# Kernel optimization log

Measured on AMD Instinct MI355X. Metric: run time of the kernel, lower is better.

Reference implementation:

```python
import jax, jax.numpy as jnp
import numpy as np


def setup_inputs() -> dict:
    key = jax.random.key(0)
    ks = jax.random.split(key, 7)
    n, L = 8, 1024
    s = 64            # input_size_1 = input_size_2 = 64
    d = s + 1         # 65, after bias-ones concat / h feature size
    inp = {
        "layer1": jax.random.normal(ks[0], (n, L, s), dtype=jnp.float32),
        "layer2": jax.random.normal(ks[1], (n, L, s), dtype=jnp.float32),
        "layer3": jax.random.normal(ks[2], (n, L, s), dtype=jnp.float32),
        "h1": jax.random.normal(ks[3], (n, L, d), dtype=jnp.float32),
        "h2": jax.random.normal(ks[4], (n, L, d), dtype=jnp.float32),
        "h3": jax.random.normal(ks[5], (n, L, d), dtype=jnp.float32),
        # quartic core W (xavier-normal-ish scale): shape (s1+1, s2+1, s2+1, s2+1)
        "W": jax.random.normal(ks[6], (d, d, d, d), dtype=jnp.float32) * 0.02,
    }
    return inp


def reference(layer1, layer2, layer3, h1, h2, h3, W):
    # Non-factorized, flag=True, 3D-input path of Qriaffine.forward:
    #   out = einsum('nia,abcd,njb,nic,njd->nij', [layer1;1], W, [layer2;1], h1, h2)
    # layer3 / h3 are unused in this branch (but layer3 is still concatenated
    # with ones in the original code, a no-op for the output).
    n, L, _ = layer1.shape
    ones = jnp.ones((n, L, 1), dtype=layer1.dtype)
    l1 = jnp.concatenate([layer1, ones], axis=-1)  # [n, L, d]
    l2 = jnp.concatenate([layer2, ones], axis=-1)  # [n, L, d]
    # efficient contraction order, avoiding the huge [n,L,d,d,d] intermediate:
    p = l1[..., :, None] * h1[..., None, :]          # niac: [n, L, d, d]
    q = jnp.einsum('niac,abcd->nibd', p, W)          # [n, L, d, d]
    r = l2[..., :, None] * h2[..., None, :]          # njbd: [n, L, d, d]
    out = jnp.einsum('nibd,njbd->nij', q, r)         # [n, L, L]
    return out
```

## Files before the change

kernel.cpp:

```cpp
#include <hip/hip_runtime.h>
#include <hip/hip_bf16.h>


typedef __attribute__((ext_vector_type(8))) short short8;
typedef __attribute__((ext_vector_type(16))) float floatx16;

#define KP 4288
#define DP 4352
#define NROW 8192

__device__ __forceinline__ void async_ld16(const void* g, void* l) {
  __builtin_amdgcn_global_load_lds(
      (const __attribute__((address_space(1))) unsigned int*)g,
      (__attribute__((address_space(3))) unsigned int*)l, 16, 0, 0);
}

__global__ void zero_pad_wt2(__hip_bfloat16* __restrict__ Wt2) {
  const int ROWPAD = 127 * KP;
  const int COLPAD = 4225 * 63;
  const int total = ROWPAD + COLPAD;
  const __hip_bfloat16 z = __float2bfloat16(0.f);
  for (int id = blockIdx.x * 256 + threadIdx.x; id < total;
       id += gridDim.x * 256) {
    if (id < ROWPAD) {
      int row = 4225 + id / KP, col = id % KP;
      Wt2[(size_t)row * KP + col] = z;
    } else {
      int j = id - ROWPAD;
      int row = j / 63, col = 4225 + j % 63;
      Wt2[(size_t)row * KP + col] = z;
    }
  }
}

__global__ void build_wt2(const float* __restrict__ W, __hip_bfloat16* __restrict__ Wt2) {
  __shared__ __hip_bfloat16 tile[65 * 66];
  const int a = blockIdx.x, b = blockIdx.y;
  const float* src = W + (size_t)(a * 65 + b) * 4225;
  for (int idx = threadIdx.x; idx < 4225; idx += 256) {
    int c = idx / 65, d = idx - c * 65;
    tile[d * 66 + c] = __float2bfloat16(src[idx]);
  }
  __syncthreads();
  for (int idx = threadIdx.x; idx < 4225; idx += 256) {
    int d = idx / 65, c = idx - d * 65;
    Wt2[(size_t)(b * 65 + d) * KP + a * 65 + c] = tile[d * 66 + c];
  }
}

__global__ void build_p(const float* __restrict__ layer, const float* __restrict__ h,
                        __hip_bfloat16* __restrict__ P, int width) {
  const int row0 = blockIdx.x * 4;
  __shared__ float lv[4][65], hv[4][65];
  for (int i = threadIdx.x; i < 260; i += 256) {
    int rr = i / 65, x = i - rr * 65;
    lv[rr][x] = (x < 64) ? layer[(size_t)(row0 + rr) * 64 + x] : 1.0f;
    hv[rr][x] = h[(size_t)(row0 + rr) * 65 + x];
  }
  __syncthreads();
#pragma unroll
  for (int rr = 0; rr < 4; ++rr) {
    const size_t rowbase = (size_t)(row0 + rr) * width;
    for (int base = threadIdx.x * 8; base < width; base += 256 * 8) {
      alignas(16) __hip_bfloat16 tmp[8];
#pragma unroll
      for (int j = 0; j < 8; ++j) {
        int idx = base + j;
        float v = 0.f;
        if (idx < 4225) {
          int x = idx / 65, y = idx - x * 65;
          v = lv[rr][x] * hv[rr][y];
        }
        tmp[j] = __float2bfloat16(v);
      }
      *(float4*)(P + rowbase + base) = *(const float4*)tmp;
    }
  }
}

template <int STORE_BF16, int SWZ>
__global__ __launch_bounds__(256) void gemm_nt(
    const __hip_bfloat16* __restrict__ A, const __hip_bfloat16* __restrict__ B,
    void* __restrict__ Cv, int K, int lda, int ldb, int ldc,
    long sA, long sB, long sC) {
  __shared__ alignas(16) __hip_bfloat16 As[128 * 64];
  __shared__ alignas(16) __hip_bfloat16 Bs[128 * 64];
  int bx = blockIdx.x, by = blockIdx.y, z = blockIdx.z;
  if (SWZ == 1) {
    int orig = blockIdx.x + 34 * blockIdx.y;
    int xcd = orig & 7;
    int idx = orig >> 3;
    int xg = (idx < 216) ? (idx / 72) : 3;
    int r = idx - xg * 72;
    bx = xg * 9 + (r >> 3);
    by = (xcd << 3) + (r & 7);
  } else if (SWZ == 2) {
    int orig = blockIdx.x + 8 * blockIdx.y + 64 * blockIdx.z;
    z = orig & 7;
    int r = orig >> 3;
    bx = r & 7;
    by = r >> 3;
  }
  A += (long)z * sA;
  B += (long)z * sB;
  const int bm = by * 128;
  const int bn = bx * 128;
  const int t = threadIdx.x;
  const int lane = t & 63;
  const int wave = t >> 6;
  const int l31 = lane & 31;
  const int lhi = lane >> 5;
  const int wm = (wave >> 1) * 64;
  const int wn = (wave & 1) * 64;

  const __hip_bfloat16* gA[4];
  const __hip_bfloat16* gB[4];
  __hip_bfloat16* lA[4];
  __hip_bfloat16* lB[4];
#pragma unroll
  for (int r = 0; r < 4; ++r) {
    int L = r * 256 + t;
    int row = L >> 3, sl = L & 7;
    int sg = sl ^ (row & 7);
    gA[r] = A + (size_t)(bm + row) * lda + sg * 8;
    gB[r] = B + (size_t)(bn + row) * ldb + sg * 8;
    lA[r] = As + (size_t)(r * 256 + wave * 64) * 8;
    lB[r] = Bs + (size_t)(r * 256 + wave * 64) * 8;
  }

  const int x7 = l31 & 7;
  const int rA0 = (wm + l31) * 64, rA1 = (wm + 32 + l31) * 64;
  const int rB0 = (wn + l31) * 64, rB1 = (wn + 32 + l31) * 64;

  floatx16 acc[2][2] = {};

  for (int k0 = 0; k0 < K; k0 += 64) {
    __syncthreads();
#pragma unroll
    for (int r = 0; r < 4; ++r) {
      async_ld16(gA[r] + k0, lA[r]);
      async_ld16(gB[r] + k0, lB[r]);
    }
    __syncthreads();

#pragma unroll
    for (int ks = 0; ks < 4; ++ks) {
      const int pc = ((ks * 2 + lhi) ^ x7) * 8;
      short8 a0 = *(const short8*)(&As[rA0 + pc]);
      short8 a1 = *(const short8*)(&As[rA1 + pc]);
      short8 b0 = *(const short8*)(&Bs[rB0 + pc]);
      short8 b1 = *(const short8*)(&Bs[rB1 + pc]);
      acc[0][0] = __builtin_amdgcn_mfma_f32_32x32x16_bf16(a0, b0, acc[0][0], 0, 0, 0);
      acc[0][1] = __builtin_amdgcn_mfma_f32_32x32x16_bf16(a0, b1, acc[0][1], 0, 0, 0);
      acc[1][0] = __builtin_amdgcn_mfma_f32_32x32x16_bf16(a1, b0, acc[1][0], 0, 0, 0);
      acc[1][1] = __builtin_amdgcn_mfma_f32_32x32x16_bf16(a1, b1, acc[1][1], 0, 0, 0);
    }
  }

  if (STORE_BF16) {
    __hip_bfloat16* C = (__hip_bfloat16*)Cv + (long)z * sC;
#pragma unroll
    for (int mt = 0; mt < 2; ++mt)
#pragma unroll
      for (int nt = 0; nt < 2; ++nt)
#pragma unroll
        for (int reg = 0; reg < 16; ++reg) {
          int row = bm + wm + mt * 32 + (reg & 3) + 8 * (reg >> 2) + 4 * lhi;
          int col = bn + wn + nt * 32 + l31;
          C[(size_t)row * ldc + col] = __float2bfloat16(acc[mt][nt][reg]);
        }
  } else {
    float* C = (float*)Cv + (long)z * sC;
#pragma unroll
    for (int mt = 0; mt < 2; ++mt)
#pragma unroll
      for (int nt = 0; nt < 2; ++nt)
#pragma unroll
        for (int reg = 0; reg < 16; ++reg) {
          int row = bm + wm + mt * 32 + (reg & 3) + 8 * (reg >> 2) + 4 * lhi;
          int col = bn + wn + nt * 32 + l31;
          C[(size_t)row * ldc + col] = acc[mt][nt][reg];
        }
  }
}

extern "C" void kernel_launch(void* const* d_in, const int* in_sizes, int n_in,
                              void* d_out, int out_size, void* d_ws, size_t ws_size,
                              hipStream_t stream) {
  const float* layer1 = (const float*)d_in[0];
  const float* layer2 = (const float*)d_in[1];
  const float* h1 = (const float*)d_in[3];
  const float* h2 = (const float*)d_in[4];
  const float* W = (const float*)d_in[6];
  float* out = (float*)d_out;

  char* ws = (char*)d_ws;
  __hip_bfloat16* P = (__hip_bfloat16*)(ws);
  __hip_bfloat16* Wt2 = (__hip_bfloat16*)(ws + 70254592ULL);
  __hip_bfloat16* Q = (__hip_bfloat16*)(ws + 107577344ULL);
  __hip_bfloat16* R = (__hip_bfloat16*)(ws);

  zero_pad_wt2<<<1024, 256, 0, stream>>>(Wt2);
  build_wt2<<<dim3(65, 65), 256, 0, stream>>>(W, Wt2);
  build_p<<<NROW / 4, 256, 0, stream>>>(layer1, h1, P, KP);
  gemm_nt<1, 1><<<dim3(DP / 128, NROW / 128, 1), 256, 0, stream>>>(
      P, Wt2, Q, KP, KP, KP, DP, 0, 0, 0);
  build_p<<<NROW / 4, 256, 0, stream>>>(layer2, h2, R, DP);
  gemm_nt<0, 2><<<dim3(1024 / 128, 1024 / 128, 8), 256, 0, stream>>>(
      Q, R, out, 4288, DP, DP, 1024, 1024L * DP, 1024L * DP, 1024L * 1024);
}
```

Before: 579.4 us.

## Replace first GEMM with 256x256-tile, 8-wave, double-buffered pipelined kernel

The large P×Wt2 GEMM moves to a new kernel that uses 256x256 output tiles with 512 threads (8 waves) and double-buffered LDS split into halves. Prefetches for the next K-steps are interleaved with four MFMA phases, using explicit barriers, vmcnt waits, sched_barrier and setprio to overlap global-to-LDS loads with compute. An XCD-aware block swizzle is kept for L2 locality. The larger tiles raise data reuse per block but use 128KB of LDS and many registers, which limits occupancy and makes correctness depend on the hand-written wait counts.

```diff
diff --git a/kernel.cpp b/kernel.cpp
--- a/kernel.cpp
+++ b/kernel.cpp
@@ -78,6 +78,161 @@
   }
 }
 
+#define SBAR __builtin_amdgcn_sched_barrier(0)
+
+__global__ __launch_bounds__(512) void gemm1_8p(
+    const __hip_bfloat16* __restrict__ A, const __hip_bfloat16* __restrict__ B,
+    __hip_bfloat16* __restrict__ C, int K, int lda, int ldb, int ldc) {
+  __shared__ alignas(16) __hip_bfloat16 As[2][2][128 * 64];
+  __shared__ alignas(16) __hip_bfloat16 Bs[2][2][128 * 64];
+  const int orig = blockIdx.x + 17 * blockIdx.y;
+  const int xcd = orig & 7;
+  const int idx = orig >> 3;
+  const int by = (xcd << 2) + idx / 17;
+  const int bx = idx % 17;
+  const int bm = by * 256, bn = bx * 256;
+
+  const int t = threadIdx.x;
+  const int lane = t & 63, w = t >> 6;
+  const int l31 = lane & 31, lhi = lane >> 5, x7 = l31 & 7;
+  const int ah = w >> 2;
+  const int wm = ah * 128;
+  const int wn = (w & 3) * 64;
+  const int bh = (w & 3) >> 1;
+  const int wnin = wn & 127;
+
+  int co[4];
+#pragma unroll
+  for (int ks = 0; ks < 4; ++ks) co[ks] = ((ks * 2 + lhi) ^ x7) * 8;
+  const int ab = l31 * 64;
+  const int bb0 = (wnin + l31) * 64;
+  const int bb1 = (wnin + 32 + l31) * 64;
+
+  const int srow = t >> 3;
+  const int sg = (t & 7) ^ (srow & 7);
+  const __hip_bfloat16* gA0 = A + (size_t)(bm + srow) * lda + sg * 8;
+  const __hip_bfloat16* gA1 = A + (size_t)(bm + 64 + srow) * lda + sg * 8;
+  const __hip_bfloat16* gB0 = B + (size_t)(bn + srow) * ldb + sg * 8;
+  const __hip_bfloat16* gB1 = B + (size_t)(bn + 64 + srow) * ldb + sg * 8;
+  const int st0 = w * 512;
+  const int st1 = 4096 + w * 512;
+
+#define STAGE_AH(kt, h)                                                        \
+  do {                                                                         \
+    const int _c = (kt) & 1;                                                   \
+    const size_t _hk = (size_t)(h) * 128 * lda + (size_t)(kt) * 64;            \
+    async_ld16(gA0 + _hk, &As[_c][h][st0]);                                    \
+    async_ld16(gA1 + _hk, &As[_c][h][st1]);                                    \
+  } while (0)
+#define STAGE_BH(kt, h)                                                        \
+  do {                                                                         \
+    const int _c = (kt) & 1;                                                   \
+    const size_t _hk = (size_t)(h) * 128 * ldb + (size_t)(kt) * 64;            \
+    async_ld16(gB0 + _hk, &Bs[_c][h][st0]);                                    \
+    async_ld16(gB1 + _hk, &Bs[_c][h][st1]);                                    \
+  } while (0)
+
+  const int NT = K >> 6;
+
+  STAGE_BH(0, 0); STAGE_BH(0, 1); STAGE_AH(0, 0); STAGE_AH(0, 1);
+  STAGE_BH(1, 0); STAGE_AH(1, 0); STAGE_AH(1, 1);
+  SBAR;
+  asm volatile("s_waitcnt vmcnt(6)\n\ts_barrier" ::: "memory");
+
+  floatx16 acc[4][2] = {};
+
+  for (int kt = 0; kt < NT; ++kt) {
+    const int c = kt & 1;
+    const __hip_bfloat16* Ah = &As[c][ah][0];
+    const __hip_bfloat16* Bh = &Bs[c][bh][0];
+    short8 bf[2][4], a0[4], a1[4], a2[4], a3[4];
+
+#pragma unroll
+    for (int ks = 0; ks < 4; ++ks) {
+      bf[0][ks] = *(const short8*)(Bh + bb0 + co[ks]);
+      bf[1][ks] = *(const short8*)(Bh + bb1 + co[ks]);
+      a0[ks] = *(const short8*)(Ah + ab + co[ks]);
+      a1[ks] = *(const short8*)(Ah + 2048 + ab + co[ks]);
+    }
+    if (kt + 1 < NT) STAGE_BH(kt + 1, 1);
+    SBAR;
+    asm volatile("s_barrier\n\ts_waitcnt lgkmcnt(0)" ::: "memory");
+    SBAR;
+    __builtin_amdgcn_s_setprio(1);
+#pragma unroll
+    for (int ks = 0; ks < 4; ++ks) {
+      acc[0][0] = __builtin_amdgcn_mfma_f32_32x32x16_bf16(a0[ks], bf[0][ks], acc[0][0], 0, 0, 0);
+      acc[0][1] = __builtin_amdgcn_mfma_f32_32x32x16_bf16(a0[ks], bf[1][ks], acc[0][1], 0, 0, 0);
+    }
+    __builtin_amdgcn_s_setprio(0);
+    SBAR;
+    asm volatile("s_barrier" ::: "memory");
+
+#pragma unroll
+    for (int ks = 0; ks < 4; ++ks) {
+      a2[ks] = *(const short8*)(Ah + 2 * 2048 + ab + co[ks]);
+      a3[ks] = *(const short8*)(Ah + 3 * 2048 + ab + co[ks]);
+    }
+    if (kt + 2 < NT) STAGE_BH(kt + 2, 0);
+    SBAR;
+    asm volatile("s_barrier\n\ts_waitcnt lgkmcnt(0)" ::: "memory");
+    SBAR;
+    __builtin_amdgcn_s_setprio(1);
+#pragma unroll
+    for (int ks = 0; ks < 4; ++ks) {
+      acc[1][0] = __builtin_amdgcn_mfma_f32_32x32x16_bf16(a1[ks], bf[0][ks], acc[1][0], 0, 0, 0);
+      acc[1][1] = __builtin_amdgcn_mfma_f32_32x32x16_bf16(a1[ks], bf[1][ks], acc[1][1], 0, 0, 0);
+    }
+    __builtin_amdgcn_s_setprio(0);
+    SBAR;
+    asm volatile("s_barrier" ::: "memory");
+
+    if (kt + 2 < NT) STAGE_AH(kt + 2, 0);
+    SBAR;
+    asm volatile("s_barrier" ::: "memory");
+    SBAR;
+    __builtin_amdgcn_s_setprio(1);
+#pragma unroll
+    for (int ks = 0; ks < 4; ++ks) {
+      acc[2][0] = __builtin_amdgcn_mfma_f32_32x32x16_bf16(a2[ks], bf[0][ks], acc[2][0], 0, 0, 0);
+      acc[2][1] = __builtin_amdgcn_mfma_f32_32x32x16_bf16(a2[ks], bf[1][ks], acc[2][1], 0, 0, 0);
+    }
+    __builtin_amdgcn_s_setprio(0);
+    SBAR;
+    asm volatile("s_barrier" ::: "memory");
+
+    if (kt + 2 < NT) STAGE_AH(kt + 2, 1);
+    SBAR;
+    if (kt < NT - 2)
+      asm volatile("s_waitcnt vmcnt(6)\n\ts_barrier" ::: "memory");
+    else
+      asm volatile("s_waitcnt vmcnt(0)\n\ts_barrier" ::: "memory");
+    SBAR;
+    __builtin_amdgcn_s_setprio(1);
+#pragma unroll
+    for (int ks = 0; ks < 4; ++ks) {
+      acc[3][0] = __builtin_amdgcn_mfma_f32_32x32x16_bf16(a3[ks], bf[0][ks], acc[3][0], 0, 0, 0);
+      acc[3][1] = __builtin_amdgcn_mfma_f32_32x32x16_bf16(a3[ks], bf[1][ks], acc[3][1], 0, 0, 0);
+    }
+    __builtin_amdgcn_s_setprio(0);
+    SBAR;
+    asm volatile("s_barrier" ::: "memory");
+  }
+
+#pragma unroll
+  for (int mf = 0; mf < 4; ++mf)
+#pragma unroll
+    for (int nf = 0; nf < 2; ++nf)
+#pragma unroll
+      for (int reg = 0; reg < 16; ++reg) {
+        int row = bm + wm + mf * 32 + (reg & 3) + 8 * (reg >> 2) + 4 * lhi;
+        int col = bn + wn + nf * 32 + l31;
+        C[(size_t)row * ldc + col] = __float2bfloat16(acc[mf][nf][reg]);
+      }
+#undef STAGE_AH
+#undef STAGE_BH
+}
+
 template <int STORE_BF16, int SWZ>
 __global__ __launch_bounds__(256) void gemm_nt(
     const __hip_bfloat16* __restrict__ A, const __hip_bfloat16* __restrict__ B,
@@ -86,15 +241,7 @@
   __shared__ alignas(16) __hip_bfloat16 As[128 * 64];
   __shared__ alignas(16) __hip_bfloat16 Bs[128 * 64];
   int bx = blockIdx.x, by = blockIdx.y, z = blockIdx.z;
-  if (SWZ == 1) {
-    int orig = blockIdx.x + 34 * blockIdx.y;
-    int xcd = orig & 7;
-    int idx = orig >> 3;
-    int xg = (idx < 216) ? (idx / 72) : 3;
-    int r = idx - xg * 72;
-    bx = xg * 9 + (r >> 3);
-    by = (xcd << 3) + (r & 7);
-  } else if (SWZ == 2) {
+  if (SWZ == 2) {
     int orig = blockIdx.x + 8 * blockIdx.y + 64 * blockIdx.z;
     z = orig & 7;
     int r = orig >> 3;
@@ -203,8 +350,8 @@
   zero_pad_wt2<<<1024, 256, 0, stream>>>(Wt2);
   build_wt2<<<dim3(65, 65), 256, 0, stream>>>(W, Wt2);
   build_p<<<NROW / 4, 256, 0, stream>>>(layer1, h1, P, KP);
-  gemm_nt<1, 1><<<dim3(DP / 128, NROW / 128, 1), 256, 0, stream>>>(
-      P, Wt2, Q, KP, KP, KP, DP, 0, 0, 0);
+  gemm1_8p<<<dim3(DP / 256, NROW / 256), 512, 0, stream>>>(
+      P, Wt2, Q, KP, KP, KP, DP);
   build_p<<<NROW / 4, 256, 0, stream>>>(layer2, h2, R, DP);
   gemm_nt<0, 2><<<dim3(1024 / 128, 1024 / 128, 8), 256, 0, stream>>>(
       Q, R, out, 4288, DP, DP, 1024, 1024L * DP, 1024L * DP, 1024L * 1024);
```

New measurement: 630.4 us. 1.09x slower.
